# Performance work log

Measured on AMD Instinct MI355X. Metric: run time of the kernel, lower is better.

The kernel has to match this reference:

```python
import jax, jax.numpy as jnp
import numpy as np

N_NODES = 10000
N_EDGES = 320000
F = 128
N_RBF = 20


def setup_inputs() -> dict:
    key = jax.random.key(0)
    ks = jax.random.split(key, 12)
    inp = {
        "idx_i": jax.random.randint(ks[0], (N_EDGES,), 0, N_NODES),
        "idx_j": jax.random.randint(ks[1], (N_EDGES,), 0, N_NODES),
        "rel_dir": jax.random.normal(ks[2], (N_EDGES, 3), dtype=jnp.float32),
        "rel_dist_cut": jax.random.uniform(ks[3], (N_EDGES,), dtype=jnp.float32),
        "rbf_features": jax.random.normal(ks[4], (N_EDGES, N_RBF), dtype=jnp.float32),
        "scalar_features": jax.random.normal(ks[5], (N_NODES, F), dtype=jnp.float32),
        "vector_features": jax.random.normal(ks[6], (N_NODES, F, 3), dtype=jnp.float32),
        # learned params: scalar_network = Linear(F,F) -> SiLU -> Linear(F,3F); rbf_network = Linear(N_RBF,3F)
        "W1": jax.random.normal(ks[7], (F, F), dtype=jnp.float32) / np.sqrt(F),
        "b1": jnp.zeros((F,), dtype=jnp.float32),
        "W2": jax.random.normal(ks[8], (F, 3 * F), dtype=jnp.float32) / np.sqrt(F),
        "b2": jnp.zeros((3 * F,), dtype=jnp.float32),
        "Wr": jax.random.normal(ks[9], (N_RBF, 3 * F), dtype=jnp.float32) / np.sqrt(N_RBF),
        "br": jnp.zeros((3 * F,), dtype=jnp.float32),
    }
    return inp


def reference(idx_i, idx_j, rel_dir, rel_dist_cut, rbf_features,
              scalar_features, vector_features, W1, b1, W2, b2, Wr, br):
    num_nodes, num_features = scalar_features.shape
    # per-node MLP: [N, 3F]
    phi = jax.nn.silu(scalar_features @ W1 + b1) @ W2 + b2
    # distance gate: [E, 3F]
    Wg = (rbf_features @ Wr + br) * rel_dist_cut[:, None]
    # gather neighbor phi and gate
    phi_W = phi[idx_j] * Wg                       # [E, 3F]
    phi_W_vv = phi_W[:, :num_features]            # [E, F]
    phi_W_ss = phi_W[:, num_features:2 * num_features]
    phi_W_vs = phi_W[:, 2 * num_features:]
    # per-receiver edge counts (bincount)
    counts = jax.ops.segment_sum(jnp.ones((idx_i.shape[0],), phi_W.dtype),
                                 idx_i, num_segments=num_nodes)  # [N]
    scalar_residuals = jax.ops.segment_sum(phi_W_ss, idx_i, num_segments=num_nodes)
    scalar_residuals = scalar_residuals / counts[:, None]
    # per-edge vector message: [E, F, 3]
    v_edge = (vector_features[idx_j] * phi_W_vv[:, :, None]
              + phi_W_vs[:, :, None] * rel_dir[:, None, :])
    vector_residuals = jax.ops.segment_sum(v_edge, idx_i, num_segments=num_nodes)
    vector_residuals = vector_residuals / counts[:, None, None]
    return (scalar_features + scalar_residuals,
            vector_features + vector_residuals)
```

## Files before the change

### kernel.cpp

```cpp
#include <hip/hip_runtime.h>
#include <hip/hip_bf16.h>

#define NN 10000
#define NE 320000
#define FDIM 128
#define NRBF 20
#define PHI_DIM 384
#define NBUCK 4
#define NKEY (NN * NBUCK)
#define SCAN_BLOCKS 157

typedef unsigned int uint;
typedef unsigned short ushort;

#if __has_builtin(__builtin_amdgcn_fdot2_f32_bf16)
#define USE_DOT2 1
typedef __bf16 bf16x2 __attribute__((ext_vector_type(2)));
#else
#define USE_DOT2 0
#endif

__device__ __forceinline__ ushort f2bf(float x) {
  __hip_bfloat16 b = __float2bfloat16(x);
  return *(ushort*)&b;
}
__device__ __forceinline__ float bflo(uint u) { return __uint_as_float(u << 16); }
__device__ __forceinline__ float bfhi(uint u) { return __uint_as_float(u & 0xffff0000u); }
__device__ __forceinline__ int jbucket(int j) { return (int)(((uint)j * NBUCK) / NN); }


__global__ __launch_bounds__(256) void phi_kernel(
    const float* __restrict__ S, const float* __restrict__ W1, const float* __restrict__ b1,
    const float* __restrict__ W2, const float* __restrict__ b2, const float* __restrict__ vf,
    const int* __restrict__ idx_i, const int* __restrict__ idx_j, int* __restrict__ counts,
    char* __restrict__ tab) {
  __shared__ float s_s[8][FDIM];
  __shared__ float h_s[8][FDIM];
  const int t = threadIdx.x;
  const int tf = t & 127;
  const int half = t >> 7;
  const int nb = blockIdx.x * 8 + half * 4;
  const int row0 = half * 4;
  {
    const int e = blockIdx.x * 256 + t;
    atomicAdd(&counts[jbucket(idx_j[e]) * NN + idx_i[e]], 1);
  }
#pragma unroll
  for (int n = 0; n < 4; n++) s_s[row0 + n][tf] = S[(nb + n) * FDIM + tf];
  __syncthreads();
  float acc[4];
#pragma unroll
  for (int n = 0; n < 4; n++) acc[n] = 0.f;
  for (int k = 0; k < FDIM; k++) {
    float w = W1[k * FDIM + tf];
#pragma unroll
    for (int n = 0; n < 4; n++) acc[n] += s_s[row0 + n][k] * w;
  }
  float bb = b1[tf];
#pragma unroll
  for (int n = 0; n < 4; n++) {
    float x = acc[n] + bb;
    h_s[row0 + n][tf] = x / (1.0f + expf(-x));
  }
  __syncthreads();
  float a0[4], a1[4], a2[4];
#pragma unroll
  for (int n = 0; n < 4; n++) { a0[n] = 0.f; a1[n] = 0.f; a2[n] = 0.f; }
  for (int k = 0; k < FDIM; k++) {
    float w0 = W2[k * PHI_DIM + tf];
    float w1 = W2[k * PHI_DIM + tf + 128];
    float w2 = W2[k * PHI_DIM + tf + 256];
#pragma unroll
    for (int n = 0; n < 4; n++) {
      float hv = h_s[row0 + n][k];
      a0[n] += hv * w0;
      a1[n] += hv * w1;
      a2[n] += hv * w2;
    }
  }
  float c0 = b2[tf], c1 = b2[tf + 128], c2 = b2[tf + 256];
#pragma unroll
  for (int n = 0; n < 4; n++) {
    const int node = nb + n;
    const float p0 = a0[n] + c0;
    const float p1 = a1[n] + c1;
    const float p2 = a2[n] + c2;
    const float* src = vf + (size_t)node * (FDIM * 3) + tf * 3;
    const uint wx = f2bf(src[0] * p0);
    const uint wy = f2bf(src[1] * p0);
    const uint wz = f2bf(src[2] * p0);
    char* pb = tab + (size_t)node * 1280;
    ((uint*)pb)[tf] = (wy << 16) | wx;
    ((uint*)(pb + 512))[tf] = ((uint)f2bf(p1) << 16) | wz;
    ((ushort*)(pb + 1024))[tf] = f2bf(p2);
  }
}

__global__ void scan1_kernel(const int* __restrict__ counts, int* __restrict__ offsets,
                             int* __restrict__ blocksums) {
  __shared__ int s[256];
  const int t = threadIdx.x;
  const int idx = blockIdx.x * 256 + t;
  const int c = counts[idx];
  s[t] = c;
  __syncthreads();
  for (int off = 1; off < 256; off <<= 1) {
    int v = (t >= off) ? s[t - off] : 0;
    __syncthreads();
    s[t] += v;
    __syncthreads();
  }
  if (idx < NKEY) offsets[idx] = s[t] - c;
  if (t == 255) blocksums[blockIdx.x] = s[255];
}

__global__ void scan2_kernel(int* __restrict__ blocksums, int* __restrict__ offsets) {
  __shared__ int s[256];
  const int t = threadIdx.x;
  int v0 = (t < SCAN_BLOCKS) ? blocksums[t] : 0;
  s[t] = v0;
  __syncthreads();
  for (int off = 1; off < 256; off <<= 1) {
    int v = (t >= off) ? s[t - off] : 0;
    __syncthreads();
    s[t] += v;
    __syncthreads();
  }
  if (t < SCAN_BLOCKS) blocksums[t] = s[t] - v0;
  if (t == 255) offsets[NKEY] = s[t];
}

__global__ void stage_kernel(const int* __restrict__ idx_i, const int* __restrict__ idx_j,
                             const float* __restrict__ cut, const float* __restrict__ dir,
                             const float* __restrict__ rbf, const int* __restrict__ offsets,
                             const int* __restrict__ blocksums, int* __restrict__ counts,
                             uint* __restrict__ edata, int* __restrict__ jlist) {
  int e = blockIdx.x * blockDim.x + threadIdx.x;
  if (e >= NE) return;
  const int j = idx_j[e];
  const int key = jbucket(j) * NN + idx_i[e];
  int pos = atomicSub(&counts[key], 1) - 1;
  const int slot = offsets[key] + blocksums[key >> 8] + pos;
  jlist[slot] = j;
  const float c = cut[e];
  uint w[12];
  w[0] = ((uint)f2bf(dir[e * 3 + 1]) << 16) | f2bf(dir[e * 3 + 0]);
  const float* rb = rbf + (size_t)e * NRBF;
#pragma unroll
  for (int r = 0; r < 10; r++) {
    uint lo = (uint)f2bf(rb[2 * r] * c);
    uint hi = (uint)f2bf(rb[2 * r + 1] * c);
    w[1 + r] = (hi << 16) | lo;
  }
  w[11] = ((uint)f2bf(dir[e * 3 + 2]) << 16) | f2bf(c);
  uint4* d = (uint4*)(edata + (size_t)slot * 12);
  d[0] = make_uint4(w[0], w[1], w[2], w[3]);
  d[1] = make_uint4(w[4], w[5], w[6], w[7]);
  d[2] = make_uint4(w[8], w[9], w[10], w[11]);
}

__global__ __launch_bounds__(128, 5) void node_kernel(
    const uint* __restrict__ edata, const int* __restrict__ jlist,
    const float* __restrict__ Wr, const float* __restrict__ br,
    const char* __restrict__ tab, const float* __restrict__ sf,
    const float* __restrict__ vf, const int* __restrict__ offsets,
    const int* __restrict__ blocksums, float* __restrict__ out) {
  const int f = threadIdx.x;
#if USE_DOT2
  bf16x2 wrA[11], wrB[11], wrC[11];
#pragma unroll
  for (int r = 0; r < 10; r++) {
    uint a = ((uint)f2bf(Wr[(2 * r + 1) * PHI_DIM + f]) << 16) | f2bf(Wr[(2 * r) * PHI_DIM + f]);
    uint b = ((uint)f2bf(Wr[(2 * r + 1) * PHI_DIM + f + 128]) << 16) |
             f2bf(Wr[(2 * r) * PHI_DIM + f + 128]);
    uint c = ((uint)f2bf(Wr[(2 * r + 1) * PHI_DIM + f + 256]) << 16) |
             f2bf(Wr[(2 * r) * PHI_DIM + f + 256]);
    wrA[r] = __builtin_bit_cast(bf16x2, a);
    wrB[r] = __builtin_bit_cast(bf16x2, b);
    wrC[r] = __builtin_bit_cast(bf16x2, c);
  }
  wrA[10] = __builtin_bit_cast(bf16x2, (uint)f2bf(br[f]));
  wrB[10] = __builtin_bit_cast(bf16x2, (uint)f2bf(br[f + 128]));
  wrC[10] = __builtin_bit_cast(bf16x2, (uint)f2bf(br[f + 256]));
#else
  float wrA[22], wrB[22], wrC[22];
#pragma unroll
  for (int r = 0; r < NRBF; r++) {
    wrA[r] = Wr[r * PHI_DIM + f];
    wrB[r] = Wr[r * PHI_DIM + f + 128];
    wrC[r] = Wr[r * PHI_DIM + f + 256];
  }
  wrA[20] = br[f];       wrA[21] = 0.f;
  wrB[20] = br[f + 128]; wrB[21] = 0.f;
  wrC[20] = br[f + 256]; wrC[21] = 0.f;
#endif
  const int n = blockIdx.x;
  const int f4 = f * 4;
  float ss = 0.f, ax = 0.f, ay = 0.f, az = 0.f;
  int cnt = 0;

  auto process = [&](uint4 e0, uint4 e1, uint4 e2, uint d0, uint d1, uint zu) {
    uint rbp[11] = {e0.y, e0.z, e0.w, e1.x, e1.y, e1.z, e1.w, e2.x, e2.y, e2.z, e2.w};
    const float dx = bflo(e0.x);
    const float dy = bfhi(e0.x);
    const float dz = bfhi(rbp[10]);
    float g0 = 0.f, g1 = 0.f, g2 = 0.f;
#if USE_DOT2
#pragma unroll
    for (int r = 0; r < 11; r++) {
      bf16x2 rp = __builtin_bit_cast(bf16x2, rbp[r]);
      g0 = __builtin_amdgcn_fdot2_f32_bf16(rp, wrA[r], g0, false);
      g1 = __builtin_amdgcn_fdot2_f32_bf16(rp, wrB[r], g1, false);
      g2 = __builtin_amdgcn_fdot2_f32_bf16(rp, wrC[r], g2, false);
    }
#else
#pragma unroll
    for (int r = 0; r < 11; r++) {
      float rlo = bflo(rbp[r]);
      float rhi = bfhi(rbp[r]);
      g0 += rlo * wrA[2 * r] + rhi * wrA[2 * r + 1];
      g1 += rlo * wrB[2 * r] + rhi * wrB[2 * r + 1];
      g2 += rlo * wrC[2 * r] + rhi * wrC[2 * r + 1];
    }
#endif
    const float vs = bflo(zu) * g2;
    ss += bfhi(d1) * g1;
    ax += bflo(d0) * g0 + vs * dx;
    ay += bfhi(d0) * g0 + vs * dy;
    az += bflo(d1) * g0 + vs * dz;
  };

  for (int b = 0; b < NBUCK; b++) {
    const int k0 = b * NN + n;
    const int beg = __builtin_amdgcn_readfirstlane(offsets[k0] + blocksums[k0 >> 8]);
    const int k1 = k0 + 1;
    const int end = __builtin_amdgcn_readfirstlane(
        (k1 < NKEY) ? (offsets[k1] + blocksums[k1 >> 8]) : offsets[NKEY]);
    cnt += end - beg;
    int p = beg;
    for (; p + 2 <= end; p += 2) {
      const int j0 = __builtin_amdgcn_readfirstlane(jlist[p]);
      const int j1 = __builtin_amdgcn_readfirstlane(jlist[p + 1]);
      const char* B0 = tab + (size_t)j0 * 1280;
      const char* B1 = tab + (size_t)j1 * 1280;
      const uint d00 = *(const uint*)(B0 + f4), d01 = *(const uint*)(B0 + 512 + f4);
      const uint z0 = *(const ushort*)(B0 + 1024 + f * 2);
      const uint d10 = *(const uint*)(B1 + f4), d11 = *(const uint*)(B1 + 512 + f4);
      const uint z1 = *(const ushort*)(B1 + 1024 + f * 2);
      const uint4* r0 = (const uint4*)(edata + (size_t)p * 12);
      const uint4* r1 = (const uint4*)(edata + (size_t)(p + 1) * 12);
      uint4 a0 = r0[0], a1 = r0[1], a2 = r0[2];
      uint4 b0 = r1[0], b1 = r1[1], b2 = r1[2];
      process(a0, a1, a2, d00, d01, z0);
      process(b0, b1, b2, d10, d11, z1);
    }
    if (p < end) {
      const int j0 = __builtin_amdgcn_readfirstlane(jlist[p]);
      const char* B0 = tab + (size_t)j0 * 1280;
      const uint d00 = *(const uint*)(B0 + f4), d01 = *(const uint*)(B0 + 512 + f4);
      const uint z0 = *(const ushort*)(B0 + 1024 + f * 2);
      const uint4* r0 = (const uint4*)(edata + (size_t)p * 12);
      process(r0[0], r0[1], r0[2], d00, d01, z0);
    }
  }

  const float inv = 1.0f / (float)cnt;
  out[(size_t)n * FDIM + f] = sf[(size_t)n * FDIM + f] + ss * inv;
  float* ov = out + (size_t)NN * FDIM + (size_t)n * (FDIM * 3) + f * 3;
  const float* iv = vf + (size_t)n * (FDIM * 3) + f * 3;
  ov[0] = iv[0] + ax * inv;
  ov[1] = iv[1] + ay * inv;
  ov[2] = iv[2] + az * inv;
}

extern "C" void kernel_launch(void* const* d_in, const int* in_sizes, int n_in,
                              void* d_out, int out_size, void* d_ws, size_t ws_size,
                              hipStream_t stream) {
  const int* idx_i = (const int*)d_in[0];
  const int* idx_j = (const int*)d_in[1];
  const float* rel_dir = (const float*)d_in[2];
  const float* cut = (const float*)d_in[3];
  const float* rbf = (const float*)d_in[4];
  const float* sf = (const float*)d_in[5];
  const float* vf = (const float*)d_in[6];
  const float* W1 = (const float*)d_in[7];
  const float* b1 = (const float*)d_in[8];
  const float* W2 = (const float*)d_in[9];
  const float* b2 = (const float*)d_in[10];
  const float* Wr = (const float*)d_in[11];
  const float* br = (const float*)d_in[12];
  float* out = (float*)d_out;

  char* w = (char*)d_ws;
  int* counts = (int*)w;
  int* offsets = (int*)(w + 163840);
  int* blocksums = (int*)(w + 327680);
  uint* edata = (uint*)(w + 328704);
  char* tab = w + 15688704;
  int* jlist = (int*)(w + 28488704);

  hipMemsetAsync(w, 0, 163840, stream);
  hipLaunchKernelGGL(phi_kernel, dim3(NN / 8), dim3(256), 0, stream, sf, W1, b1, W2, b2, vf,
                     idx_i, idx_j, counts, tab);
  hipLaunchKernelGGL(scan1_kernel, dim3(SCAN_BLOCKS), dim3(256), 0, stream, counts, offsets,
                     blocksums);
  hipLaunchKernelGGL(scan2_kernel, dim3(1), dim3(256), 0, stream, blocksums, offsets);
  hipLaunchKernelGGL(stage_kernel, dim3((NE + 255) / 256), dim3(256), 0, stream, idx_i, idx_j,
                     cut, rel_dir, rbf, offsets, blocksums, counts, edata, jlist);
  hipLaunchKernelGGL(node_kernel, dim3(NN), dim3(128), 0, stream, edata, jlist, Wr, br, tab, sf,
                     vf, offsets, blocksums, out);
}
```

Before: 153.6 us.

## Compute per-node MLP with bf16 MFMA using prepacked weight fragments

Replaces the scalar FP32 loops of the two-layer node MLP in phi_kernel with 16x16x32 bf16 MFMA instructions, processing 16 nodes per block instead of 8. A new wconv_kernel repacks W1 and W2 into bf16 fragment layouts each call, and intermediate activations and phi are staged through shared memory in bf16. This cuts the ALU-bound MLP cost and halves the phi grid, at the price of an extra launch, lower-precision MLP inputs and hidden activations, and more edges counted per thread.

```diff
diff --git a/kernel.cpp b/kernel.cpp
--- a/kernel.cpp
+++ b/kernel.cpp
@@ -12,6 +12,8 @@
 
 typedef unsigned int uint;
 typedef unsigned short ushort;
+typedef __bf16 bf16x8 __attribute__((ext_vector_type(8)));
+typedef float f32x4 __attribute__((ext_vector_type(4)));
 
 #if __has_builtin(__builtin_amdgcn_fdot2_f32_bf16)
 #define USE_DOT2 1
@@ -26,73 +28,114 @@
 }
 __device__ __forceinline__ float bflo(uint u) { return __uint_as_float(u << 16); }
 __device__ __forceinline__ float bfhi(uint u) { return __uint_as_float(u & 0xffff0000u); }
+__device__ __forceinline__ float bf2f(ushort u) { return __uint_as_float(((uint)u) << 16); }
 __device__ __forceinline__ int jbucket(int j) { return (int)(((uint)j * NBUCK) / NN); }
 
 
+__global__ void wconv_kernel(const float* __restrict__ W1, const float* __restrict__ W2,
+                             ushort* __restrict__ W1p, ushort* __restrict__ W2p) {
+  const int gid = blockIdx.x * 256 + threadIdx.x;
+  if (gid < 2048) {
+    const int n = gid & 127, g = (gid >> 7) & 3, ks = gid >> 9;
+    ushort* dst = W1p + gid * 8;
+#pragma unroll
+    for (int e = 0; e < 8; e++) dst[e] = f2bf(W1[(ks * 32 + g * 8 + e) * FDIM + n]);
+  } else {
+    const int q = gid - 2048;
+    const int ks = q / 1536;
+    const int rem = q - ks * 1536;
+    const int g = rem / 384;
+    const int n = rem - g * 384;
+    ushort* dst = W2p + q * 8;
+#pragma unroll
+    for (int e = 0; e < 8; e++) dst[e] = f2bf(W2[(ks * 32 + g * 8 + e) * PHI_DIM + n]);
+  }
+}
+
 __global__ __launch_bounds__(256) void phi_kernel(
-    const float* __restrict__ S, const float* __restrict__ W1, const float* __restrict__ b1,
-    const float* __restrict__ W2, const float* __restrict__ b2, const float* __restrict__ vf,
-    const int* __restrict__ idx_i, const int* __restrict__ idx_j, int* __restrict__ counts,
+    const float* __restrict__ S, const float* __restrict__ b1, const float* __restrict__ b2,
+    const float* __restrict__ vf, const int* __restrict__ idx_i, const int* __restrict__ idx_j,
+    int* __restrict__ counts, const ushort* __restrict__ W1p, const ushort* __restrict__ W2p,
     char* __restrict__ tab) {
-  __shared__ float s_s[8][FDIM];
-  __shared__ float h_s[8][FDIM];
+  __shared__ ushort Hb[16][136];
+  __shared__ ushort Pb[16][392];
   const int t = threadIdx.x;
-  const int tf = t & 127;
-  const int half = t >> 7;
-  const int nb = blockIdx.x * 8 + half * 4;
-  const int row0 = half * 4;
+  const int lane = t & 63;
+  const int wv = t >> 6;
+  const int mrow = lane & 15;
+  const int kg = lane >> 4;
   {
-    const int e = blockIdx.x * 256 + t;
-    atomicAdd(&counts[jbucket(idx_j[e]) * NN + idx_i[e]], 1);
-  }
-#pragma unroll
-  for (int n = 0; n < 4; n++) s_s[row0 + n][tf] = S[(nb + n) * FDIM + tf];
+    const int e0 = (blockIdx.x * 256 + t) * 2;
+    atomicAdd(&counts[jbucket(idx_j[e0]) * NN + idx_i[e0]], 1);
+    atomicAdd(&counts[jbucket(idx_j[e0 + 1]) * NN + idx_i[e0 + 1]], 1);
+  }
+  const int n0 = blockIdx.x * 16;
+  bf16x8 sfrag[4];
+#pragma unroll
+  for (int ks = 0; ks < 4; ks++) {
+    const float* sp = S + (size_t)(n0 + mrow) * FDIM + ks * 32 + kg * 8;
+    float4 v0 = *(const float4*)sp;
+    float4 v1 = *(const float4*)(sp + 4);
+    uint w0 = ((uint)f2bf(v0.y) << 16) | f2bf(v0.x);
+    uint w1 = ((uint)f2bf(v0.w) << 16) | f2bf(v0.z);
+    uint w2 = ((uint)f2bf(v1.y) << 16) | f2bf(v1.x);
+    uint w3 = ((uint)f2bf(v1.w) << 16) | f2bf(v1.z);
+    sfrag[ks] = __builtin_bit_cast(bf16x8, make_uint4(w0, w1, w2, w3));
+  }
+#pragma unroll
+  for (int tile = 0; tile < 2; tile++) {
+    const int nc = wv * 32 + tile * 16 + mrow;
+    f32x4 acc = {0.f, 0.f, 0.f, 0.f};
+#pragma unroll
+    for (int ks = 0; ks < 4; ks++) {
+      bf16x8 bfrag = __builtin_bit_cast(
+          bf16x8, *(const uint4*)(W1p + ((size_t)(ks * 4 + kg) * FDIM + nc) * 8));
+      acc = __builtin_amdgcn_mfma_f32_16x16x32_bf16(sfrag[ks], bfrag, acc, 0, 0, 0);
+    }
+    const float bb = b1[nc];
+#pragma unroll
+    for (int r = 0; r < 4; r++) {
+      const float x = acc[r] + bb;
+      Hb[kg * 4 + r][nc] = f2bf(x / (1.0f + expf(-x)));
+    }
+  }
   __syncthreads();
-  float acc[4];
-#pragma unroll
-  for (int n = 0; n < 4; n++) acc[n] = 0.f;
-  for (int k = 0; k < FDIM; k++) {
-    float w = W1[k * FDIM + tf];
-#pragma unroll
-    for (int n = 0; n < 4; n++) acc[n] += s_s[row0 + n][k] * w;
-  }
-  float bb = b1[tf];
-#pragma unroll
-  for (int n = 0; n < 4; n++) {
-    float x = acc[n] + bb;
-    h_s[row0 + n][tf] = x / (1.0f + expf(-x));
+  bf16x8 hfrag[4];
+#pragma unroll
+  for (int ks = 0; ks < 4; ks++)
+    hfrag[ks] = __builtin_bit_cast(bf16x8, *(const uint4*)&Hb[mrow][ks * 32 + kg * 8]);
+#pragma unroll
+  for (int tile = 0; tile < 6; tile++) {
+    const int nc = wv * 96 + tile * 16 + mrow;
+    f32x4 acc = {0.f, 0.f, 0.f, 0.f};
+#pragma unroll
+    for (int ks = 0; ks < 4; ks++) {
+      bf16x8 bfrag = __builtin_bit_cast(
+          bf16x8, *(const uint4*)(W2p + ((size_t)(ks * 4 + kg) * PHI_DIM + nc) * 8));
+      acc = __builtin_amdgcn_mfma_f32_16x16x32_bf16(hfrag[ks], bfrag, acc, 0, 0, 0);
+    }
+    const float bb = b2[nc];
+#pragma unroll
+    for (int r = 0; r < 4; r++) Pb[kg * 4 + r][nc] = f2bf(acc[r] + bb);
   }
   __syncthreads();
-  float a0[4], a1[4], a2[4];
-#pragma unroll
-  for (int n = 0; n < 4; n++) { a0[n] = 0.f; a1[n] = 0.f; a2[n] = 0.f; }
-  for (int k = 0; k < FDIM; k++) {
-    float w0 = W2[k * PHI_DIM + tf];
-    float w1 = W2[k * PHI_DIM + tf + 128];
-    float w2 = W2[k * PHI_DIM + tf + 256];
-#pragma unroll
-    for (int n = 0; n < 4; n++) {
-      float hv = h_s[row0 + n][k];
-      a0[n] += hv * w0;
-      a1[n] += hv * w1;
-      a2[n] += hv * w2;
-    }
-  }
-  float c0 = b2[tf], c1 = b2[tf + 128], c2 = b2[tf + 256];
-#pragma unroll
-  for (int n = 0; n < 4; n++) {
-    const int node = nb + n;
-    const float p0 = a0[n] + c0;
-    const float p1 = a1[n] + c1;
-    const float p2 = a2[n] + c2;
-    const float* src = vf + (size_t)node * (FDIM * 3) + tf * 3;
+#pragma unroll
+  for (int c = 0; c < 8; c++) {
+    const int idx = c * 256 + t;
+    const int nd = idx >> 7;
+    const int f = idx & 127;
+    const int node = n0 + nd;
+    const float p0 = bf2f(Pb[nd][f]);
+    const uint p1u = Pb[nd][f + 128];
+    const ushort p2u = Pb[nd][f + 256];
+    const float* src = vf + (size_t)node * (FDIM * 3) + f * 3;
     const uint wx = f2bf(src[0] * p0);
     const uint wy = f2bf(src[1] * p0);
     const uint wz = f2bf(src[2] * p0);
     char* pb = tab + (size_t)node * 1280;
-    ((uint*)pb)[tf] = (wy << 16) | wx;
-    ((uint*)(pb + 512))[tf] = ((uint)f2bf(p1) << 16) | wz;
-    ((ushort*)(pb + 1024))[tf] = f2bf(p2);
+    ((uint*)pb)[f] = (wy << 16) | wx;
+    ((uint*)(pb + 512))[f] = (p1u << 16) | wz;
+    ((ushort*)(pb + 1024))[f] = p2u;
   }
 }
 
@@ -298,10 +341,13 @@
   uint* edata = (uint*)(w + 328704);
   char* tab = w + 15688704;
   int* jlist = (int*)(w + 28488704);
+  ushort* W1p = (ushort*)(w + 29768704);
+  ushort* W2p = (ushort*)(w + 29801472);
 
   hipMemsetAsync(w, 0, 163840, stream);
-  hipLaunchKernelGGL(phi_kernel, dim3(NN / 8), dim3(256), 0, stream, sf, W1, b1, W2, b2, vf,
-                     idx_i, idx_j, counts, tab);
+  hipLaunchKernelGGL(wconv_kernel, dim3(32), dim3(256), 0, stream, W1, W2, W1p, W2p);
+  hipLaunchKernelGGL(phi_kernel, dim3(NN / 16), dim3(256), 0, stream, sf, b1, b2, vf, idx_i,
+                     idx_j, counts, W1p, W2p, tab);
   hipLaunchKernelGGL(scan1_kernel, dim3(SCAN_BLOCKS), dim3(256), 0, stream, counts, offsets,
                      blocksums);
   hipLaunchKernelGGL(scan2_kernel, dim3(1), dim3(256), 0, stream, blocksums, offsets);
```

Measured after the change: 137.2 us, median of 5. -10.7%, faster.
